# Optimization experiments

Measured on AMD Instinct MI355X. Metric: run time of the kernel, lower is better.

## Reference

```python
import jax, jax.numpy as jnp
import numpy as np

B, N, DIM = 64, 64, 256
HEADS, P = 4, 16
H, W, C = 56, 56, 256
CH = C // HEADS            # per-head channels = eff_in_dim = eff_out_dim = 64
IN_PTS = HEADS * P         # 64
OUT_PTS = IN_PTS           # 64
TOTAL = CH * CH + IN_PTS * OUT_PTS  # 8192
GRAD_NORM = 1.0 / H

# RestrictGradNorm: identity fwd, clamp grad in bwd
@jax.custom_vjp
def restrict_grad(x):
    return x

def _rg_fwd(x):
    return x, None

def _rg_bwd(_, g):
    return (jnp.clip(g, -GRAD_NORM, GRAD_NORM),)

restrict_grad.defvjp(_rg_fwd, _rg_bwd)


def grid_sample_bilinear(feat, grid):
    # feat [G,c,h,w], grid [G,Hg,Wg,2] in [-1,1]; align_corners=False, zeros padding
    G, c, h, w = feat.shape
    Hg, Wg = grid.shape[1], grid.shape[2]
    Q = Hg * Wg
    x = (grid[..., 0] + 1.0) * 0.5 * w - 0.5
    y = (grid[..., 1] + 1.0) * 0.5 * h - 0.5
    x0f = jnp.floor(x); y0f = jnp.floor(y)
    wx1 = x - x0f; wx0 = 1.0 - wx1
    wy1 = y - y0f; wy0 = 1.0 - wy1
    x0 = x0f.astype(jnp.int32); y0 = y0f.astype(jnp.int32)
    fflat = feat.reshape(G, c, h * w)

    def gather(xi, yi):
        valid = (xi >= 0) & (xi < w) & (yi >= 0) & (yi < h)
        idx = (jnp.clip(yi, 0, h - 1) * w + jnp.clip(xi, 0, w - 1)).reshape(G, Q)
        v = jnp.take_along_axis(fflat, jnp.broadcast_to(idx[:, None, :], (G, c, Q)), axis=2)
        return v * valid.reshape(G, 1, Q)

    out = (gather(x0, y0) * (wx0 * wy0).reshape(G, 1, Q)
           + gather(x0 + 1, y0) * (wx1 * wy0).reshape(G, 1, Q)
           + gather(x0, y0 + 1) * (wx0 * wy1).reshape(G, 1, Q)
           + gather(x0 + 1, y0 + 1) * (wx1 * wy1).reshape(G, 1, Q))
    return out.reshape(G, c, Hg, Wg)


def setup_inputs() -> dict:
    key = jax.random.key(0)
    ks = jax.random.split(key, 10)
    img_feat = jax.random.normal(ks[0], (B, C, H, W), jnp.float32)
    ctr = jax.random.uniform(ks[1], (B, N, 2), jnp.float32) * 0.8 + 0.1
    wh = jax.random.uniform(ks[2], (B, N, 2), jnp.float32) * 0.4 + 0.1
    token_roi = jnp.concatenate([ctr - wh / 2, ctr + wh / 2], axis=-1)
    query = jax.random.normal(ks[3], (B, N, DIM), jnp.float32)
    W_off = jax.random.normal(ks[4], (DIM, HEADS * P * 2), jnp.float32) * 0.02
    b_off = jnp.zeros((HEADS * P * 2,), jnp.float32)
    ln_w = jnp.ones((DIM,), jnp.float32)
    ln_b = jnp.zeros((DIM,), jnp.float32)
    W1 = jax.random.normal(ks[5], (DIM, DIM // 4), jnp.float32) * 0.02
    b1 = jnp.zeros((DIM // 4,), jnp.float32)
    W2 = jax.random.normal(ks[6], (DIM // 4, TOTAL), jnp.float32) * 0.02
    b2 = jax.random.normal(ks[7], (TOTAL,), jnp.float32) * 0.02
    m_beta = jnp.zeros((CH,), jnp.float32)
    s_beta = jnp.zeros((OUT_PTS,), jnp.float32)
    W_out = jax.random.normal(ks[8], (CH * OUT_PTS, DIM), jnp.float32) * 0.02
    b_out = jnp.zeros((DIM,), jnp.float32)
    return dict(img_feat=img_feat, token_roi=token_roi, query=query, W_off=W_off,
                b_off=b_off, ln_w=ln_w, ln_b=ln_b, W1=W1, b1=b1, W2=W2, b2=b2,
                m_beta=m_beta, s_beta=s_beta, W_out=W_out, b_out=b_out)


def _forward(img_feat, token_roi, query, W_off, b_off, ln_w, ln_b, W1, b1, W2, b2,
             m_beta, s_beta, W_out, b_out):
    # 1) sampling offsets from query
    off = (query @ W_off + b_off).reshape(B, N, 1, IN_PTS, 2)
    # 2) make_absolute_sampling_point: normalize over points (unbiased std, as torch)
    mean = off.mean(axis=-2, keepdims=True)
    std = jnp.std(off, axis=-2, ddof=1, keepdims=True) + 1e-7
    off = (off - mean) / (3.0 * std)
    roi_xy = (token_roi[:, :, 2:] + token_roi[:, :, :2]) * 0.5   # [B,N,2]
    roi_wh = token_roi[:, :, 2:] - token_roi[:, :, :2]
    pts = roi_xy[:, :, None, None, :] + off * roi_wh[:, :, None, None, :]  # [B,N,1,HP,2]
    # 3) sampling_from_img_feat: per-head bilinear grid sample
    sp = pts.reshape(B, N, 1, HEADS, P, 2).transpose(0, 3, 1, 2, 4, 5)
    sp = sp.reshape(B * HEADS, N, P, 2)
    sp = restrict_grad(sp)
    grid = sp * 2.0 - 1.0
    feat = img_feat.reshape(B * HEADS, CH, H, W)
    out = grid_sample_bilinear(feat, grid)                        # [B*HEADS, CH, N, P]
    out = out.reshape(B, HEADS, CH, N, 1, P).transpose(0, 3, 4, 1, 5, 2)
    sampled = out.reshape(B * N, IN_PTS, CH)                      # g==1 in AdaptiveMixing
    # 4) AdaptiveMixing: parameter generator (LN eps 1e-6 -> Linear -> Linear)
    mu = query.mean(-1, keepdims=True)
    var = query.var(-1, keepdims=True)
    qn = (query - mu) / jnp.sqrt(var + 1e-6) * ln_w + ln_b
    params = ((qn @ W1 + b1) @ W2 + b2).reshape(B * N, TOTAL)
    cm = params[:, :CH * CH].reshape(B * N, CH, CH)               # channel mixing
    sm = params[:, CH * CH:].reshape(B * N, OUT_PTS, IN_PTS)      # spatial mixing
    x = jax.nn.gelu(jnp.einsum('bpc,bcd->bpd', sampled, cm) + m_beta, approximate=False)
    x = jax.nn.gelu(jnp.einsum('bop,bpc->boc', sm, x) + s_beta[None, :, None], approximate=False)
    x = x.reshape(B, N, OUT_PTS * CH) @ W_out + b_out
    return x


def reference(img_feat, token_roi, query, W_off, b_off, ln_w, ln_b, W1, b1, W2, b2,
              m_beta, s_beta, W_out, b_out):
    return _forward(img_feat, token_roi, query, W_off, b_off, ln_w, ln_b, W1, b1,
                    W2, b2, m_beta, s_beta, W_out, b_out)
```

## Files before the change

kernel.cpp:

```cpp
#include <hip/hip_runtime.h>


typedef unsigned short u16;
typedef u16 u16x8 __attribute__((ext_vector_type(8)));
typedef short bf16x8 __attribute__((ext_vector_type(8)));
typedef float f32x4 __attribute__((ext_vector_type(4)));
#define SA 72
#define MFMA(a, b, c) __builtin_amdgcn_mfma_f32_16x16x32_bf16(a, b, c, 0, 0, 0)

static __device__ __forceinline__ float bf2f(u16 s) {
    union { float f; unsigned u; } v; v.u = ((unsigned)s) << 16; return v.f;
}
static __device__ __forceinline__ u16 f2bf(float f) {
    union { float f; unsigned u; } v; v.f = f;
    unsigned r = v.u + 0x7fffu + ((v.u >> 16) & 1u);
    return (u16)(r >> 16);
}
static __device__ __forceinline__ float gelu(float x) {
    return 0.5f * x * (1.0f + erff(x * 0.70710678118654752f));
}
static __device__ __forceinline__ float loadf(const void* p, size_t i, int isbf) {
    return isbf ? bf2f(((const u16*)p)[i]) : ((const float*)p)[i];
}

__global__ void kdetect(const void* __restrict__ lnw, int* __restrict__ flag) {
    if (threadIdx.x == 0) {
        unsigned v = *(const unsigned*)lnw;
        *flag = (v == 0x3F800000u) ? 0 : 1;
    }
}

__global__ void ktrans_bf(const void* __restrict__ src, u16* __restrict__ dst,
                          int R, int C, const int* __restrict__ flag) {
    __shared__ __align__(16) float tile[64 * 65];
    const int c0 = blockIdx.x * 64, r0 = blockIdx.y * 64;
    const int tid = threadIdx.x;
    const int isbf = *flag;
#pragma unroll
    for (int i = 0; i < 16; i++) {
        int e = i * 256 + tid;
        int rr = e >> 6, cc = e & 63;
        tile[rr * 65 + cc] = loadf(src, (size_t)(r0 + rr) * C + c0 + cc, isbf);
    }
    __syncthreads();
#pragma unroll
    for (int i = 0; i < 16; i++) {
        int e = i * 256 + tid;
        int cc = e >> 6, rr = e & 63;
        dst[(size_t)(c0 + cc) * R + r0 + rr] = f2bf(tile[rr * 65 + cc]);
    }
}

__global__ void k0_transpose(const void* __restrict__ img, u16* __restrict__ featT,
                             const int* __restrict__ flag) {
    __shared__ __align__(16) float tile[64 * 65];
    const int pos0 = blockIdx.x * 64, c0 = blockIdx.y * 64, bz = blockIdx.z;
    const int tid = threadIdx.x;
    const int isbf = *flag;
#pragma unroll
    for (int i = 0; i < 16; i++) {
        int e = i * 256 + tid;
        int cy = e >> 6, px = e & 63;
        tile[cy * 65 + px] = loadf(img, ((size_t)bz * 256 + c0 + cy) * 3136 + pos0 + px, isbf);
    }
    __syncthreads();
#pragma unroll
    for (int i = 0; i < 16; i++) {
        int e = i * 256 + tid;
        int cy = e & 63, px = e >> 6;
        featT[((size_t)bz * 3136 + pos0 + px) * 256 + c0 + cy] = f2bf(tile[cy * 65 + px]);
    }
}

__global__ void k1_points(const void* __restrict__ query, const void* __restrict__ roi,
                          const void* __restrict__ W_off, const void* __restrict__ b_off,
                          const void* __restrict__ ln_w, const void* __restrict__ ln_b,
                          const void* __restrict__ W1, const void* __restrict__ b1,
                          const int* __restrict__ flag,
                          float* __restrict__ pts, u16* __restrict__ hbuf) {
    __shared__ float qf[256], qn[256], offl[128], red[4], stats[8];
    const int t = blockIdx.x, tid = threadIdx.x;
    const int isbf = *flag;
    float q = loadf(query, (size_t)t * 256 + tid, isbf);
    qf[tid] = q;
    float v = q;
#pragma unroll
    for (int o = 32; o; o >>= 1) v += __shfl_down(v, o, 64);
    if ((tid & 63) == 0) red[tid >> 6] = v;
    __syncthreads();
    if (tid == 0) stats[0] = (red[0] + red[1] + red[2] + red[3]) * (1.f / 256.f);
    __syncthreads();
    float mu = stats[0];
    float dv = q - mu;
    v = dv * dv;
#pragma unroll
    for (int o = 32; o; o >>= 1) v += __shfl_down(v, o, 64);
    if ((tid & 63) == 0) red[tid >> 6] = v;
    __syncthreads();
    if (tid == 0) stats[1] = (red[0] + red[1] + red[2] + red[3]) * (1.f / 256.f);
    __syncthreads();
    float inv = rsqrtf(stats[1] + 1e-6f);
    qn[tid] = dv * inv * loadf(ln_w, tid, isbf) + loadf(ln_b, tid, isbf);
    __syncthreads();
    if (tid < 128) {
        float a = loadf(b_off, tid, isbf);
        for (int d = 0; d < 256; d++) a = fmaf(qf[d], loadf(W_off, (size_t)d * 128 + tid, isbf), a);
        offl[tid] = a;
    } else if (tid < 192) {
        int k = tid - 128;
        float a = loadf(b1, k, isbf);
        for (int d = 0; d < 256; d++) a = fmaf(qn[d], loadf(W1, (size_t)d * 64 + k, isbf), a);
        hbuf[(size_t)t * 64 + k] = f2bf(a);
    }
    __syncthreads();
    if (tid < 2) {
        float m = 0.f;
        for (int p = 0; p < 64; p++) m += offl[p * 2 + tid];
        m *= (1.f / 64.f);
        float s2 = 0.f;
        for (int p = 0; p < 64; p++) { float d = offl[p * 2 + tid] - m; s2 += d * d; }
        float sd = sqrtf(s2 * (1.f / 63.f));
        stats[2 + tid] = m;
        stats[4 + tid] = 1.f / (3.f * (sd + 1e-7f));
    }
    __syncthreads();
    if (tid < 128) {
        int xy = tid & 1;
        float lo = loadf(roi, (size_t)t * 4 + xy, isbf);
        float hi = loadf(roi, (size_t)t * 4 + 2 + xy, isbf);
        float ctr = 0.5f * (lo + hi), wh = hi - lo;
        pts[(size_t)t * 128 + tid] = ctr + (offl[tid] - stats[2 + xy]) * stats[4 + xy] * wh;
    }
}

__global__ void k2_sample_t(const u16* __restrict__ featT, const float* __restrict__ pts,
                            u16* __restrict__ sampled) {
    const int t = blockIdx.x, tid = threadIdx.x;
    const int pt = tid >> 2, cg = tid & 3;
    const int b = t >> 6, hh = pt >> 4;
    const float px = pts[(size_t)t * 128 + pt * 2], py = pts[(size_t)t * 128 + pt * 2 + 1];
    const float x = px * 56.f - 0.5f, y = py * 56.f - 0.5f;
    const float x0f = floorf(x), y0f = floorf(y);
    const int ix0 = (int)x0f, iy0 = (int)y0f;
    const float wx1 = x - x0f, wx0 = 1.f - wx1, wy1 = y - y0f, wy0 = 1.f - wy1;
    float acc[16];
#pragma unroll
    for (int i = 0; i < 16; i++) acc[i] = 0.f;
    const int chbase = hh * 64 + cg * 16;
#pragma unroll
    for (int corner = 0; corner < 4; corner++) {
        const int xi = ix0 + (corner & 1), yi = iy0 + (corner >> 1);
        const float wgt = ((corner & 1) ? wx1 : wx0) * ((corner >> 1) ? wy1 : wy0);
        if (xi >= 0 && xi < 56 && yi >= 0 && yi < 56) {
            const u16x8* p8 = (const u16x8*)&featT[((size_t)b * 3136 + yi * 56 + xi) * 256 + chbase];
            u16x8 a = p8[0], c = p8[1];
#pragma unroll
            for (int i = 0; i < 8; i++) {
                acc[i]     = fmaf(wgt, bf2f(a[i]), acc[i]);
                acc[8 + i] = fmaf(wgt, bf2f(c[i]), acc[8 + i]);
            }
        }
    }
    u16x8 o0, o1;
#pragma unroll
    for (int i = 0; i < 8; i++) { o0[i] = f2bf(acc[i]); o1[i] = f2bf(acc[8 + i]); }
    u16x8* q8 = (u16x8*)&sampled[(size_t)t * 4096 + pt * 64 + cg * 16];
    q8[0] = o0; q8[1] = o1;
}

__global__ void k2_sample_d(const void* __restrict__ img, const float* __restrict__ pts,
                            u16* __restrict__ sampled, const int* __restrict__ flag) {
    const int t = blockIdx.x, tid = threadIdx.x;
    const int pt = tid >> 2, cg = tid & 3;
    const int b = t >> 6, hh = pt >> 4;
    const int isbf = *flag;
    const float px = pts[(size_t)t * 128 + pt * 2], py = pts[(size_t)t * 128 + pt * 2 + 1];
    const float x = px * 56.f - 0.5f, y = py * 56.f - 0.5f;
    const float x0f = floorf(x), y0f = floorf(y);
    const int ix0 = (int)x0f, iy0 = (int)y0f;
    const float wx1 = x - x0f, wx0 = 1.f - wx1, wy1 = y - y0f, wy0 = 1.f - wy1;
    float acc[16];
#pragma unroll
    for (int i = 0; i < 16; i++) acc[i] = 0.f;
    const int chbase = b * 256 + hh * 64 + cg * 16;
#pragma unroll
    for (int corner = 0; corner < 4; corner++) {
        const int xi = ix0 + (corner & 1), yi = iy0 + (corner >> 1);
        const float wgt = ((corner & 1) ? wx1 : wx0) * ((corner >> 1) ? wy1 : wy0);
        if (xi >= 0 && xi < 56 && yi >= 0 && yi < 56) {
            const size_t sp = yi * 56 + xi;
#pragma unroll
            for (int i = 0; i < 16; i++)
                acc[i] = fmaf(wgt, loadf(img, ((size_t)(chbase + i)) * 3136 + sp, isbf), acc[i]);
        }
    }
    for (int i = 0; i < 16; i++)
        sampled[(size_t)t * 4096 + pt * 64 + cg * 16 + i] = f2bf(acc[i]);
}

__global__ __launch_bounds__(256) void k4_mfma(const u16* __restrict__ hb,
        const u16* __restrict__ W2T, const void* __restrict__ b2,
        const int* __restrict__ flag, u16* __restrict__ params) {
    __shared__ u16 As[64 * SA];
    __shared__ u16 Bs[64 * SA];
    const int tid = threadIdx.x;
    const int m0 = blockIdx.x * 64, n0 = blockIdx.y * 64;
    const int isbf = *flag;
    const int lane = tid & 63, w = tid >> 6;
    const int wm = w & 1, wn = w >> 1;
    const int l16 = lane & 15, quad = lane >> 4;
    {
        const int row = tid >> 2, kp = (tid & 3) * 16;
        const u16x8* ga = (const u16x8*)&hb[(size_t)(m0 + row) * 64 + kp];
        *(u16x8*)&As[row * SA + kp]     = ga[0];
        *(u16x8*)&As[row * SA + kp + 8] = ga[1];
        const u16x8* gb = (const u16x8*)&W2T[(size_t)(n0 + row) * 64 + kp];
        *(u16x8*)&Bs[row * SA + kp]     = gb[0];
        *(u16x8*)&Bs[row * SA + kp + 8] = gb[1];
    }
    __syncthreads();
    f32x4 acc[2][2];
#pragma unroll
    for (int i = 0; i < 2; i++)
#pragma unroll
        for (int j = 0; j < 2; j++) acc[i][j] = (f32x4){0.f, 0.f, 0.f, 0.f};
#pragma unroll
    for (int kk = 0; kk < 64; kk += 32) {
        bf16x8 af[2], bfr[2];
        af[0]  = *(const bf16x8*)&As[(wm * 32 + l16) * SA + kk + quad * 8];
        af[1]  = *(const bf16x8*)&As[(wm * 32 + 16 + l16) * SA + kk + quad * 8];
        bfr[0] = *(const bf16x8*)&Bs[(wn * 32 + l16) * SA + kk + quad * 8];
        bfr[1] = *(const bf16x8*)&Bs[(wn * 32 + 16 + l16) * SA + kk + quad * 8];
#pragma unroll
        for (int tm = 0; tm < 2; tm++)
#pragma unroll
            for (int tn = 0; tn < 2; tn++)
                acc[tm][tn] = MFMA(af[tm], bfr[tn], acc[tm][tn]);
    }
    float bb[2];
    bb[0] = loadf(b2, n0 + wn * 32 + l16, isbf);
    bb[1] = loadf(b2, n0 + wn * 32 + 16 + l16, isbf);
#pragma unroll
    for (int tm = 0; tm < 2; tm++)
#pragma unroll
        for (int tn = 0; tn < 2; tn++)
#pragma unroll
            for (int r = 0; r < 4; r++) {
                int row = m0 + wm * 32 + tm * 16 + quad * 4 + r;
                int col = n0 + wn * 32 + tn * 16 + l16;
                params[(size_t)row * 8192 + col] = f2bf(acc[tm][tn][r] + bb[tn]);
            }
}

__global__ __launch_bounds__(256) void k5_mfma(const u16* __restrict__ params,
        const void* __restrict__ m_beta, const void* __restrict__ s_beta,
        const int* __restrict__ flag, u16* __restrict__ sampled) {
    __shared__ u16 S[64 * SA];
    __shared__ u16 CMT[64 * SA];
    __shared__ u16 SM[64 * SA];
    __shared__ u16 X1T[64 * SA];
    const int t = blockIdx.x, tid = threadIdx.x;
    const int isbf = *flag;
    const size_t pbase = (size_t)t * 8192, sbase = (size_t)t * 4096;
    const int lane = tid & 63, w = tid >> 6;
    const int wm = w & 1, wn = w >> 1;
    const int l16 = lane & 15, quad = lane >> 4;
    {
        const int r = tid >> 2, cp = (tid & 3) * 16;
        const u16x8* gs = (const u16x8*)&sampled[sbase + r * 64 + cp];
        *(u16x8*)&S[r * SA + cp]     = gs[0];
        *(u16x8*)&S[r * SA + cp + 8] = gs[1];
        const u16x8* gm = (const u16x8*)&params[pbase + 4096 + r * 64 + cp];
        *(u16x8*)&SM[r * SA + cp]     = gm[0];
        *(u16x8*)&SM[r * SA + cp + 8] = gm[1];
    }
    {
        const int d = tid & 63, cp = (tid >> 6) * 16;
        u16x8 b0, b1;
#pragma unroll
        for (int j = 0; j < 8; j++) {
            b0[j] = params[pbase + (size_t)(cp + j) * 64 + d];
            b1[j] = params[pbase + (size_t)(cp + 8 + j) * 64 + d];
        }
        *(u16x8*)&CMT[d * SA + cp]     = b0;
        *(u16x8*)&CMT[d * SA + cp + 8] = b1;
    }
    __syncthreads();
    f32x4 acc[2][2];
#pragma unroll
    for (int i = 0; i < 2; i++)
#pragma unroll
        for (int j = 0; j < 2; j++) acc[i][j] = (f32x4){0.f, 0.f, 0.f, 0.f};
#pragma unroll
    for (int kk = 0; kk < 64; kk += 32) {
        bf16x8 af[2], bfr[2];
        af[0]  = *(const bf16x8*)&S[(wm * 32 + l16) * SA + kk + quad * 8];
        af[1]  = *(const bf16x8*)&S[(wm * 32 + 16 + l16) * SA + kk + quad * 8];
        bfr[0] = *(const bf16x8*)&CMT[(wn * 32 + l16) * SA + kk + quad * 8];
        bfr[1] = *(const bf16x8*)&CMT[(wn * 32 + 16 + l16) * SA + kk + quad * 8];
#pragma unroll
        for (int tm = 0; tm < 2; tm++)
#pragma unroll
            for (int tn = 0; tn < 2; tn++)
                acc[tm][tn] = MFMA(af[tm], bfr[tn], acc[tm][tn]);
    }
    float mb[2];
    mb[0] = loadf(m_beta, wn * 32 + l16, isbf);
    mb[1] = loadf(m_beta, wn * 32 + 16 + l16, isbf);
#pragma unroll
    for (int tm = 0; tm < 2; tm++)
#pragma unroll
        for (int tn = 0; tn < 2; tn++)
#pragma unroll
            for (int r = 0; r < 4; r++) {
                int p = wm * 32 + tm * 16 + quad * 4 + r;
                int d = wn * 32 + tn * 16 + l16;
                X1T[d * SA + p] = f2bf(gelu(acc[tm][tn][r] + mb[tn]));
            }
    __syncthreads();
#pragma unroll
    for (int i = 0; i < 2; i++)
#pragma unroll
        for (int j = 0; j < 2; j++) acc[i][j] = (f32x4){0.f, 0.f, 0.f, 0.f};
#pragma unroll
    for (int kk = 0; kk < 64; kk += 32) {
        bf16x8 af[2], bfr[2];
        af[0]  = *(const bf16x8*)&SM[(wm * 32 + l16) * SA + kk + quad * 8];
        af[1]  = *(const bf16x8*)&SM[(wm * 32 + 16 + l16) * SA + kk + quad * 8];
        bfr[0] = *(const bf16x8*)&X1T[(wn * 32 + l16) * SA + kk + quad * 8];
        bfr[1] = *(const bf16x8*)&X1T[(wn * 32 + 16 + l16) * SA + kk + quad * 8];
#pragma unroll
        for (int tm = 0; tm < 2; tm++)
#pragma unroll
            for (int tn = 0; tn < 2; tn++)
                acc[tm][tn] = MFMA(af[tm], bfr[tn], acc[tm][tn]);
    }
#pragma unroll
    for (int tm = 0; tm < 2; tm++)
#pragma unroll
        for (int tn = 0; tn < 2; tn++)
#pragma unroll
            for (int r = 0; r < 4; r++) {
                int o = wm * 32 + tm * 16 + quad * 4 + r;
                int d = wn * 32 + tn * 16 + l16;
                float sb = loadf(s_beta, o, isbf);
                sampled[sbase + o * 64 + d] = f2bf(gelu(acc[tm][tn][r] + sb));
            }
}

__global__ __launch_bounds__(256) void k6_mfma(const u16* __restrict__ x2b,
        const u16* __restrict__ WoutT, float* __restrict__ part) {
    __shared__ u16 As[64 * SA];
    __shared__ u16 Bs[64 * SA];
    const int tid = threadIdx.x;
    const int m0 = blockIdx.x * 64, n0 = blockIdx.y * 64, kz = blockIdx.z;
    const int lane = tid & 63, w = tid >> 6;
    const int wm = w & 1, wn = w >> 1;
    const int l16 = lane & 15, quad = lane >> 4;
    const int sRow = tid >> 2, sK = (tid & 3) * 16;
    f32x4 acc[2][2];
#pragma unroll
    for (int i = 0; i < 2; i++)
#pragma unroll
        for (int j = 0; j < 2; j++) acc[i][j] = (f32x4){0.f, 0.f, 0.f, 0.f};
    const int kbeg = kz * 2048, kend = kbeg + 2048;
    for (int k0 = kbeg; k0 < kend; k0 += 64) {
        const u16x8* ga = (const u16x8*)&x2b[(size_t)(m0 + sRow) * 4096 + k0 + sK];
        u16x8 a0 = ga[0], a1 = ga[1];
        const u16x8* gb = (const u16x8*)&WoutT[(size_t)(n0 + sRow) * 4096 + k0 + sK];
        u16x8 b0 = gb[0], b1 = gb[1];
        __syncthreads();
        *(u16x8*)&As[sRow * SA + sK]     = a0;
        *(u16x8*)&As[sRow * SA + sK + 8] = a1;
        *(u16x8*)&Bs[sRow * SA + sK]     = b0;
        *(u16x8*)&Bs[sRow * SA + sK + 8] = b1;
        __syncthreads();
#pragma unroll
        for (int kk = 0; kk < 64; kk += 32) {
            bf16x8 af[2], bfr[2];
            af[0]  = *(const bf16x8*)&As[(wm * 32 + l16) * SA + kk + quad * 8];
            af[1]  = *(const bf16x8*)&As[(wm * 32 + 16 + l16) * SA + kk + quad * 8];
            bfr[0] = *(const bf16x8*)&Bs[(wn * 32 + l16) * SA + kk + quad * 8];
            bfr[1] = *(const bf16x8*)&Bs[(wn * 32 + 16 + l16) * SA + kk + quad * 8];
#pragma unroll
            for (int tm = 0; tm < 2; tm++)
#pragma unroll
                for (int tn = 0; tn < 2; tn++)
                    acc[tm][tn] = MFMA(af[tm], bfr[tn], acc[tm][tn]);
        }
    }
    float* pbase = part + (size_t)kz * (4096 * 256);
#pragma unroll
    for (int tm = 0; tm < 2; tm++)
#pragma unroll
        for (int tn = 0; tn < 2; tn++)
#pragma unroll
            for (int r = 0; r < 4; r++) {
                int row = m0 + wm * 32 + tm * 16 + quad * 4 + r;
                int col = n0 + wn * 32 + tn * 16 + l16;
                pbase[(size_t)row * 256 + col] = acc[tm][tn][r];
            }
}

__global__ void k7_reduce(const float* __restrict__ part, const void* __restrict__ b_out,
                          const int* __restrict__ flag, float* __restrict__ out) {
    const int i = blockIdx.x * 256 + threadIdx.x;
    const int isbf = *flag;
    out[i] = part[i] + part[4096 * 256 + i] + loadf(b_out, i & 255, isbf);
}

extern "C" void kernel_launch(void* const* d_in, const int* in_sizes, int n_in,
                              void* d_out, int out_size, void* d_ws, size_t ws_size,
                              hipStream_t stream) {
    const void* img    = d_in[0];
    const void* roi    = d_in[1];
    const void* query  = d_in[2];
    const void* W_off  = d_in[3];
    const void* b_off  = d_in[4];
    const void* ln_w   = d_in[5];
    const void* ln_b   = d_in[6];
    const void* W1     = d_in[7];
    const void* b1     = d_in[8];
    const void* W2     = d_in[9];
    const void* b2     = d_in[10];
    const void* m_beta = d_in[11];
    const void* s_beta = d_in[12];
    const void* W_out  = d_in[13];
    const void* b_out  = d_in[14];

    char* ws = (char*)d_ws;
    int*   flag    = (int*)(ws + 0);
    float* pts     = (float*)(ws + 1024);
    u16*   hbuf    = (u16*)(ws + 2098176);
    u16*   sampled = (u16*)(ws + 2622464);
    u16*   params  = (u16*)(ws + 36176896);
    u16*   W2T     = (u16*)(ws + 103285760);
    u16*   WoutT   = (u16*)(ws + 104334336);
    float* part    = (float*)(ws + 106431488);
    u16*   featT   = (u16*)(ws + 114820096);
    const bool tierA = ws_size >= (size_t)217580544;

    kdetect<<<1, 64, 0, stream>>>(ln_w, flag);
    k1_points<<<4096, 256, 0, stream>>>(query, roi, W_off, b_off, ln_w, ln_b, W1, b1,
                                        flag, pts, hbuf);
    ktrans_bf<<<dim3(128, 1), 256, 0, stream>>>(W2, W2T, 64, 8192, flag);
    ktrans_bf<<<dim3(4, 64), 256, 0, stream>>>(W_out, WoutT, 4096, 256, flag);
    if (tierA) {
        k0_transpose<<<dim3(49, 4, 64), 256, 0, stream>>>(img, featT, flag);
        k2_sample_t<<<4096, 256, 0, stream>>>(featT, pts, sampled);
    } else {
        k2_sample_d<<<4096, 256, 0, stream>>>(img, pts, sampled, flag);
    }
    k4_mfma<<<dim3(64, 128), 256, 0, stream>>>(hbuf, W2T, b2, flag, params);
    k5_mfma<<<4096, 256, 0, stream>>>(params, m_beta, s_beta, flag, sampled);
    k6_mfma<<<dim3(64, 4, 2), 256, 0, stream>>>(sampled, WoutT, part);
    k7_reduce<<<4096, 256, 0, stream>>>(part, b_out, flag, (float*)d_out);
}
```

Measured before the change: 552.3 us.

## Approximate erf in GELU, branchless sampling, double-buffer and 4-way split-K output GEMM

Replaces erff in GELU with an Abramowitz-Stegun polynomial plus __expf, which is cheaper but less precise (about 1e-7 absolute error on erf). Bilinear sampling now clamps coordinates and zeroes the weights of out-of-range corners, so loads are issued without branches. The output GEMM double-buffers its LDS tiles and prefetches the next K slice into registers while computing, which removes one barrier per step. Its split-K factor rises from 2 to 4 for more blocks, at the cost of a larger partial buffer and a 4-way reduce.

```diff
diff --git a/kernel.cpp b/kernel.cpp
--- a/kernel.cpp
+++ b/kernel.cpp
@@ -17,7 +17,18 @@
     return (u16)(r >> 16);
 }
 static __device__ __forceinline__ float gelu(float x) {
-    return 0.5f * x * (1.0f + erff(x * 0.70710678118654752f));
+    const float z  = x * 0.70710678118654752f;
+    const float az = fabsf(z);
+    const float t  = 1.0f / fmaf(0.3275911f, az, 1.0f);
+    float p = fmaf(t, 1.061405429f, -1.453152027f);
+    p = fmaf(t, p, 1.421413741f);
+    p = fmaf(t, p, -0.284496736f);
+    p = fmaf(t, p, 0.254829592f);
+    p = p * t;
+    const float e    = __expf(-z * z);
+    const float erfa = fmaf(-p, e, 1.0f);
+    const float erfz = copysignf(erfa, z);
+    return 0.5f * x * (1.0f + erfz);
 }
 static __device__ __forceinline__ float loadf(const void* p, size_t i, int isbf) {
     return isbf ? bf2f(((const u16*)p)[i]) : ((const float*)p)[i];
@@ -150,15 +161,15 @@
 #pragma unroll
     for (int corner = 0; corner < 4; corner++) {
         const int xi = ix0 + (corner & 1), yi = iy0 + (corner >> 1);
-        const float wgt = ((corner & 1) ? wx1 : wx0) * ((corner >> 1) ? wy1 : wy0);
-        if (xi >= 0 && xi < 56 && yi >= 0 && yi < 56) {
-            const u16x8* p8 = (const u16x8*)&featT[((size_t)b * 3136 + yi * 56 + xi) * 256 + chbase];
-            u16x8 a = p8[0], c = p8[1];
-#pragma unroll
-            for (int i = 0; i < 8; i++) {
-                acc[i]     = fmaf(wgt, bf2f(a[i]), acc[i]);
-                acc[8 + i] = fmaf(wgt, bf2f(c[i]), acc[8 + i]);
-            }
+        const bool ok = (xi >= 0) & (xi < 56) & (yi >= 0) & (yi < 56);
+        const float wgt = ok ? ((corner & 1) ? wx1 : wx0) * ((corner >> 1) ? wy1 : wy0) : 0.f;
+        const int xc = min(max(xi, 0), 55), yc = min(max(yi, 0), 55);
+        const u16x8* p8 = (const u16x8*)&featT[((size_t)b * 3136 + yc * 56 + xc) * 256 + chbase];
+        u16x8 a = p8[0], c = p8[1];
+#pragma unroll
+        for (int i = 0; i < 8; i++) {
+            acc[i]     = fmaf(wgt, bf2f(a[i]), acc[i]);
+            acc[8 + i] = fmaf(wgt, bf2f(c[i]), acc[8 + i]);
         }
     }
     u16x8 o0, o1;
@@ -186,13 +197,13 @@
 #pragma unroll
     for (int corner = 0; corner < 4; corner++) {
         const int xi = ix0 + (corner & 1), yi = iy0 + (corner >> 1);
-        const float wgt = ((corner & 1) ? wx1 : wx0) * ((corner >> 1) ? wy1 : wy0);
-        if (xi >= 0 && xi < 56 && yi >= 0 && yi < 56) {
-            const size_t sp = yi * 56 + xi;
-#pragma unroll
-            for (int i = 0; i < 16; i++)
-                acc[i] = fmaf(wgt, loadf(img, ((size_t)(chbase + i)) * 3136 + sp, isbf), acc[i]);
-        }
+        const bool ok = (xi >= 0) & (xi < 56) & (yi >= 0) & (yi < 56);
+        const float wgt = ok ? ((corner & 1) ? wx1 : wx0) * ((corner >> 1) ? wy1 : wy0) : 0.f;
+        const int xc = min(max(xi, 0), 55), yc = min(max(yi, 0), 55);
+        const size_t sp = yc * 56 + xc;
+#pragma unroll
+        for (int i = 0; i < 16; i++)
+            acc[i] = fmaf(wgt, loadf(img, ((size_t)(chbase + i)) * 3136 + sp, isbf), acc[i]);
     }
     for (int i = 0; i < 16; i++)
         sampled[(size_t)t * 4096 + pt * 64 + cg * 16 + i] = f2bf(acc[i]);
@@ -350,38 +361,44 @@
 
 __global__ __launch_bounds__(256) void k6_mfma(const u16* __restrict__ x2b,
         const u16* __restrict__ WoutT, float* __restrict__ part) {
-    __shared__ u16 As[64 * SA];
-    __shared__ u16 Bs[64 * SA];
+    __shared__ u16 As[2][64 * SA];
+    __shared__ u16 Bs[2][64 * SA];
     const int tid = threadIdx.x;
     const int m0 = blockIdx.x * 64, n0 = blockIdx.y * 64, kz = blockIdx.z;
     const int lane = tid & 63, w = tid >> 6;
     const int wm = w & 1, wn = w >> 1;
     const int l16 = lane & 15, quad = lane >> 4;
     const int sRow = tid >> 2, sK = (tid & 3) * 16;
+    const u16* aRow = &x2b[(size_t)(m0 + sRow) * 4096 + kz * 1024 + sK];
+    const u16* bRow = &WoutT[(size_t)(n0 + sRow) * 4096 + kz * 1024 + sK];
     f32x4 acc[2][2];
 #pragma unroll
     for (int i = 0; i < 2; i++)
 #pragma unroll
         for (int j = 0; j < 2; j++) acc[i][j] = (f32x4){0.f, 0.f, 0.f, 0.f};
-    const int kbeg = kz * 2048, kend = kbeg + 2048;
-    for (int k0 = kbeg; k0 < kend; k0 += 64) {
-        const u16x8* ga = (const u16x8*)&x2b[(size_t)(m0 + sRow) * 4096 + k0 + sK];
-        u16x8 a0 = ga[0], a1 = ga[1];
-        const u16x8* gb = (const u16x8*)&WoutT[(size_t)(n0 + sRow) * 4096 + k0 + sK];
-        u16x8 b0 = gb[0], b1 = gb[1];
+    u16x8 ra0 = ((const u16x8*)aRow)[0], ra1 = ((const u16x8*)aRow)[1];
+    u16x8 rb0 = ((const u16x8*)bRow)[0], rb1 = ((const u16x8*)bRow)[1];
+#pragma unroll
+    for (int it = 0; it < 16; ++it) {
+        const int cur = it & 1;
+        *(u16x8*)&As[cur][sRow * SA + sK]     = ra0;
+        *(u16x8*)&As[cur][sRow * SA + sK + 8] = ra1;
+        *(u16x8*)&Bs[cur][sRow * SA + sK]     = rb0;
+        *(u16x8*)&Bs[cur][sRow * SA + sK + 8] = rb1;
         __syncthreads();
-        *(u16x8*)&As[sRow * SA + sK]     = a0;
-        *(u16x8*)&As[sRow * SA + sK + 8] = a1;
-        *(u16x8*)&Bs[sRow * SA + sK]     = b0;
-        *(u16x8*)&Bs[sRow * SA + sK + 8] = b1;
-        __syncthreads();
+        if (it + 1 < 16) {
+            const u16* an = aRow + (it + 1) * 64;
+            const u16* bn = bRow + (it + 1) * 64;
+            ra0 = ((const u16x8*)an)[0]; ra1 = ((const u16x8*)an)[1];
+            rb0 = ((const u16x8*)bn)[0]; rb1 = ((const u16x8*)bn)[1];
+        }
 #pragma unroll
         for (int kk = 0; kk < 64; kk += 32) {
             bf16x8 af[2], bfr[2];
-            af[0]  = *(const bf16x8*)&As[(wm * 32 + l16) * SA + kk + quad * 8];
-            af[1]  = *(const bf16x8*)&As[(wm * 32 + 16 + l16) * SA + kk + quad * 8];
-            bfr[0] = *(const bf16x8*)&Bs[(wn * 32 + l16) * SA + kk + quad * 8];
-            bfr[1] = *(const bf16x8*)&Bs[(wn * 32 + 16 + l16) * SA + kk + quad * 8];
+            af[0]  = *(const bf16x8*)&As[cur][(wm * 32 + l16) * SA + kk + quad * 8];
+            af[1]  = *(const bf16x8*)&As[cur][(wm * 32 + 16 + l16) * SA + kk + quad * 8];
+            bfr[0] = *(const bf16x8*)&Bs[cur][(wn * 32 + l16) * SA + kk + quad * 8];
+            bfr[1] = *(const bf16x8*)&Bs[cur][(wn * 32 + 16 + l16) * SA + kk + quad * 8];
 #pragma unroll
             for (int tm = 0; tm < 2; tm++)
 #pragma unroll
@@ -406,7 +423,8 @@
                           const int* __restrict__ flag, float* __restrict__ out) {
     const int i = blockIdx.x * 256 + threadIdx.x;
     const int isbf = *flag;
-    out[i] = part[i] + part[4096 * 256 + i] + loadf(b_out, i & 255, isbf);
+    out[i] = part[i] + part[1048576 + i] + part[2 * 1048576 + i] + part[3 * 1048576 + i]
+           + loadf(b_out, i & 255, isbf);
 }
 
 extern "C" void kernel_launch(void* const* d_in, const int* in_sizes, int n_in,
@@ -437,8 +455,8 @@
     u16*   W2T     = (u16*)(ws + 103285760);
     u16*   WoutT   = (u16*)(ws + 104334336);
     float* part    = (float*)(ws + 106431488);
-    u16*   featT   = (u16*)(ws + 114820096);
-    const bool tierA = ws_size >= (size_t)217580544;
+    u16*   featT   = (u16*)(ws + 123208704);
+    const bool tierA = ws_size >= (size_t)225969152;
 
     kdetect<<<1, 64, 0, stream>>>(ln_w, flag);
     k1_points<<<4096, 256, 0, stream>>>(query, roi, W_off, b_off, ln_w, ln_b, W1, b1,
@@ -453,6 +471,6 @@
     }
     k4_mfma<<<dim3(64, 128), 256, 0, stream>>>(hbuf, W2T, b2, flag, params);
     k5_mfma<<<4096, 256, 0, stream>>>(params, m_beta, s_beta, flag, sampled);
-    k6_mfma<<<dim3(64, 4, 2), 256, 0, stream>>>(sampled, WoutT, part);
+    k6_mfma<<<dim3(64, 4, 4), 256, 0, stream>>>(sampled, WoutT, part);
     k7_reduce<<<4096, 256, 0, stream>>>(part, b_out, flag, (float*)d_out);
 }
```

New measurement: 547.3 us. Within noise of the previous version (-0.9%).
